# Optimization experiments

Hardware: AMD Instinct MI355X
Metric: run time of the kernel (lower is better)

## Reference

```python
import jax, jax.numpy as jnp
from jax import lax
import numpy as np

B, T, D = 1024, 64, 512   # batch, obs_len, input_size
HD = 512                  # hidden_size
L = 3                     # n_layers
FN = 64                   # num_filters
OH = 1                    # output_horizon
ATTN_LEN = T - 1          # conv kernel height
FEAT = HD                 # feat_size = attn_size - filter_size + 1, filter_size=1


def setup_inputs() -> dict:
    key = jax.random.key(0)
    ks = jax.random.split(key, 12)
    s = 0.02
    x = jax.random.normal(ks[0], (B, T, D), dtype=jnp.float32)
    # stacked LSTM weights (input_size == hidden_size so layer-0 stacks cleanly)
    W_ih = jax.random.normal(ks[1], (L, 4 * HD, HD), dtype=jnp.float32) * s
    W_hh = jax.random.normal(ks[2], (L, 4 * HD, HD), dtype=jnp.float32) * s
    b_ih = jax.random.normal(ks[3], (L, 4 * HD), dtype=jnp.float32) * s
    b_hh = jax.random.normal(ks[4], (L, 4 * HD), dtype=jnp.float32) * s
    # TPA: Conv2d(1, FN, (ATTN_LEN, 1)) in torch layout [FN, 1, ATTN_LEN, 1]
    conv_W = jax.random.normal(ks[5], (FN, 1, ATTN_LEN, 1), dtype=jnp.float32) * s
    conv_b = jax.random.normal(ks[6], (FN,), dtype=jnp.float32) * s
    lin1_W = jax.random.normal(ks[7], (FN, HD), dtype=jnp.float32) * s
    lin1_b = jax.random.normal(ks[8], (FN,), dtype=jnp.float32) * s
    lin2_W = jax.random.normal(ks[9], (HD, HD + FN), dtype=jnp.float32) * s
    lin2_b = jnp.zeros((HD,), dtype=jnp.float32)
    out_W = jax.random.normal(ks[10], (OH, HD), dtype=jnp.float32) * s
    out_b = jnp.zeros((OH,), dtype=jnp.float32)
    return dict(x=x, W_ih=W_ih, W_hh=W_hh, b_ih=b_ih, b_hh=b_hh,
                conv_W=conv_W, conv_b=conv_b, lin1_W=lin1_W, lin1_b=lin1_b,
                lin2_W=lin2_W, lin2_b=lin2_b, out_W=out_W, out_b=out_b)


def _lstm_last_layer_hs(x, W_ih, W_hh, b_ih, b_hh):
    """Run L-layer LSTM over time, return last-layer hidden per step [T,B,HD]."""
    h0 = jnp.zeros((L, B, HD), x.dtype)
    c0 = jnp.zeros((L, B, HD), x.dtype)

    def step(carry, xt):
        h, c = carry  # [L,B,HD]
        inp = xt
        hs, cs = [], []
        for l in range(L):  # small fixed layer count
            gates = inp @ W_ih[l].T + h[l] @ W_hh[l].T + b_ih[l] + b_hh[l]
            i, f, g, o = jnp.split(gates, 4, axis=-1)  # torch gate order i,f,g,o
            cl = jax.nn.sigmoid(f) * c[l] + jax.nn.sigmoid(i) * jnp.tanh(g)
            hl = jax.nn.sigmoid(o) * jnp.tanh(cl)
            hs.append(hl)
            cs.append(cl)
            inp = hl
        return (jnp.stack(hs), jnp.stack(cs)), hs[-1]

    _, ys = lax.scan(step, (h0, c0), jnp.swapaxes(x, 0, 1))
    return ys  # [T,B,HD]


def reference(x, W_ih, W_hh, b_ih, b_hh, conv_W, conv_b,
              lin1_W, lin1_b, lin2_W, lin2_b, out_W, out_b):
    ys = _lstm_last_layer_hs(x, W_ih, W_hh, b_ih, b_hh)   # [T,B,HD]
    htt = ys[-1]                                          # [B,HD] final hidden
    H = jax.nn.relu(jnp.swapaxes(ys[:-1], 0, 1))          # [B,T-1,HD]

    # Conv2d(1,FN,(T-1,1)) over [B,1,T-1,HD]: contracts the time axis only
    kW = conv_W[:, 0, :, 0]                               # [FN,T-1]
    conv_bcf = jnp.einsum('btf,ct->bcf', H, kW) + conv_b[:, None]  # [B,FN,FEAT]
    # torch .view(-1, feat_size, filter_num) on contiguous [B,FN,1,FEAT]
    conv_vecs = jax.nn.relu(conv_bcf.reshape(B, FEAT, FN))         # [B,FEAT,FN]

    w = htt @ lin1_W.T + lin1_b                           # [B,FN]
    s = jnp.sum(conv_vecs * w[:, None, :], axis=2)        # [B,FEAT]
    alpha = jax.nn.sigmoid(s)
    v = jnp.sum(alpha[:, :, None] * conv_vecs, axis=1)    # [B,FN]

    concat = jnp.concatenate([htt, v], axis=1)            # [B,HD+FN]
    new_ht = concat @ lin2_W.T + lin2_b                   # [B,HD]
    ypred = (new_ht @ out_W.T + out_b)[:, :, None]        # [B,OH,1]
    return ypred
```

## Files before the change

### kernel.cpp

```cpp
#include <hip/hip_runtime.h>
#include <hip/hip_bf16.h>


typedef short v8s __attribute__((ext_vector_type(8)));
typedef float v4f __attribute__((ext_vector_type(4)));
typedef __hip_bfloat16 bf16;

#define B_   1024
#define T_   64
#define D_   512
#define HD_  512

__device__ __forceinline__ float sigm(float v) { return 1.0f / (1.0f + __expf(-v)); }
__device__ __forceinline__ float tanh_(float v) { return 2.0f / (1.0f + __expf(-2.0f * v)) - 1.0f; }
__device__ __forceinline__ float b2f(bf16 v) { return __bfloat162float(v); }
__device__ __forceinline__ float bu2f(ushort u) {
  union { unsigned i; float f; } x; x.i = ((unsigned)u) << 16; return x.f;
}

__device__ __forceinline__ void cvt_store8(ushort* dst, const float* src) {
  float4 a = *(const float4*)src;
  float4 b = *(const float4*)(src + 4);
  bf16 h[8] = {__float2bfloat16(a.x), __float2bfloat16(a.y),
               __float2bfloat16(a.z), __float2bfloat16(a.w),
               __float2bfloat16(b.x), __float2bfloat16(b.y),
               __float2bfloat16(b.z), __float2bfloat16(b.w)};
  *(uint4*)dst = *(const uint4*)h;
}

__device__ __forceinline__ void glds16(const bf16* g, ushort* l) {
  __builtin_amdgcn_global_load_lds(
      (const __attribute__((address_space(1))) void*)g,
      (__attribute__((address_space(3))) void*)l, 16, 0, 0);
}

constexpr size_t SZ_YS = (size_t)T_ * B_ * HD_ * 2;
constexpr size_t SZ_HB = (size_t)2 * 2 * B_ * HD_ * 2;
constexpr size_t SZ_CB = (size_t)3 * B_ * HD_ * 4;
constexpr size_t SZ_ZP = (size_t)B_ * HD_ * 2;
constexpr size_t SZ_WV = (size_t)B_ * 64 * 4;
constexpr size_t SZ_VB = (size_t)B_ * 64 * 4;
constexpr size_t SZ_WB = (size_t)3 * 2048 * 1024 * 2;
constexpr size_t SZ_KT = (size_t)64 * 64 * 2;
constexpr size_t SZ_FW = (size_t)640 * 4;
constexpr size_t SZ_XB = (size_t)T_ * B_ * D_ * 2;
constexpr size_t O_YS = 0;
constexpr size_t O_HB = O_YS + SZ_YS;
constexpr size_t O_CB = O_HB + SZ_HB;
constexpr size_t O_ZP = O_CB + SZ_CB;
constexpr size_t O_WV = O_ZP + SZ_ZP;
constexpr size_t O_VB = O_WV + SZ_WV;
constexpr size_t O_WB = O_VB + SZ_VB;
constexpr size_t O_KT = O_WB + SZ_WB;
constexpr size_t O_FW = O_KT + SZ_KT;
constexpr size_t O_XB = O_FW + SZ_FW;

__global__ __launch_bounds__(256) void prep_w(const float* __restrict__ Wih,
                                              const float* __restrict__ Whh,
                                              bf16* __restrict__ Wbuf) {
  int tf = blockIdx.x * 256 + threadIdx.x;
  int group = tf >> 10;
  int layer = group >> 8, rem = group & 255;
  int nt = rem >> 4, ch = rem & 15;
  int li = tf & 1023;
  int frag = li >> 6, lane = li & 63;
  int nb = frag >> 1, kk = frag & 1;
  int c = lane & 15, q = lane >> 4;
  int half = nb >> 2, gate = nb & 3;
  int j = nt * 32 + half * 16 + c;
  int R = gate * 512 + j;
  int k = (ch & 7) * 64 + kk * 32 + q * 8;
  const float* src = ((ch < 8) ? Wih : Whh) + ((size_t)layer * 2048 + R) * 512 + k;
  cvt_store8((ushort*)(Wbuf + (size_t)tf * 8), src);
}

__global__ __launch_bounds__(256) void prep_x(const float* __restrict__ x,
                                              bf16* __restrict__ xb) {
  int idx = blockIdx.x * 256 + threadIdx.x;
  int d8 = idx & 63;
  int bt = idx >> 6;
  int b = bt & 1023, t = bt >> 10;
  cvt_store8((ushort*)(xb + ((size_t)t * B_ + b) * D_ + d8 * 8),
             x + ((size_t)b * T_ + t) * D_ + d8 * 8);
}

__global__ __launch_bounds__(256) void prep_kt(const float* __restrict__ convW,
                                               bf16* __restrict__ kT) {
  int idx = blockIdx.x * 256 + threadIdx.x;
  int t = idx >> 6, c = idx & 63;
  kT[idx] = __float2bfloat16(t < 63 ? convW[c * 63 + t] : 0.f);
}

__global__ __launch_bounds__(64) void prep_fw(const float* __restrict__ lin2W,
                                              const float* __restrict__ lin2b,
                                              const float* __restrict__ outW,
                                              const float* __restrict__ outb,
                                              float* __restrict__ fw) {
  const int blk = blockIdx.x, tid = threadIdx.x;
  if (blk < 9) {
    const int k = blk * 64 + tid;
    float a = 0.f;
    for (int j = 0; j < 512; ++j) a += outW[j] * lin2W[(size_t)j * 576 + k];
    fw[k] = a;
  } else {
    float a = 0.f;
    for (int j = tid; j < 512; j += 64) a += outW[j] * lin2b[j];
    for (int m = 1; m < 64; m <<= 1) a += __shfl_xor(a, m);
    if (tid == 0) fw[576] = a + outb[0];
  }
}

__global__ __launch_bounds__(512, 6) void lstm_stage(
    const bf16* __restrict__ xb, const bf16* __restrict__ Wbuf,
    const float* __restrict__ bih, const float* __restrict__ bhh,
    bf16* __restrict__ ys, bf16* __restrict__ hbuf, float* __restrict__ cbuf,
    const bf16* __restrict__ zp, int s, int llo) {
  __shared__ ushort As[2][4096];
  __shared__ ushort Bs[2][8192];

  const int layer = llo + (blockIdx.x >> 8);
  const int tile = blockIdx.x & 255;
  const int t = s - layer;
  const int mt = tile >> 4, nt = tile & 15;
  const int b0 = mt << 6;
  const int p = s & 1;

  bf16* hw = (layer < 2) ? hbuf + ((size_t)p * 2 + layer) * (B_ * HD_)
                         : ys + (size_t)t * (B_ * HD_);
  const bf16* srcA0 = (layer == 0)
      ? xb + (size_t)t * (B_ * D_)
      : hbuf + ((size_t)(p ^ 1) * 2 + (layer - 1)) * (B_ * HD_);
  const bf16* srcA1 = (layer < 2)
      ? hbuf + ((size_t)(p ^ 1) * 2 + layer) * (B_ * HD_)
      : ((t == 0) ? zp : ys + (size_t)(t - 1) * (B_ * HD_));
  const bf16* Wb = Wbuf + ((size_t)layer * 16 + nt) * 16 * 8192;

  const int tid = threadIdx.x, lane = tid & 63, w = tid >> 6;
  const int c = lane & 15, q = lane >> 4;
  const int wm = w >> 1, wn = w & 1;

  v4f acc[4];
#pragma unroll
  for (int ni = 0; ni < 4; ++ni) acc[ni] = v4f{0.f, 0.f, 0.f, 0.f};

  auto STAGE = [&](int ch, int pb) {
    const int kof = (ch & 7) * 64;
    const bf16* wsrc = Wb + (size_t)ch * 8192;
    const bf16* sA = (ch < 8) ? srcA0 : srcA1;
#pragma unroll
    for (int i = 0; i < 3; ++i) {
      int idx = w * 3 + i;
      if (idx < 16) {
        glds16(wsrc + idx * 512 + lane * 8, &Bs[pb][idx * 512]);
      } else {
        int f = idx - 16, mb = f >> 1, k2 = f & 1;
        glds16(sA + (size_t)(b0 + mb * 16 + c) * HD_ + kof + k2 * 32 + q * 8,
               &As[pb][f * 512]);
      }
    }
  };

  STAGE(0, 0);
  __syncthreads();

  for (int ch = 0; ch < 16; ++ch) {
    const int pb = ch & 1;
    if (ch < 15) STAGE(ch + 1, pb ^ 1);
    __builtin_amdgcn_s_setprio(1);
#pragma unroll
    for (int kk = 0; kk < 2; ++kk) {
      v8s af = *(const v8s*)&As[pb][(wm * 2 + kk) * 512 + lane * 8];
#pragma unroll
      for (int ni = 0; ni < 4; ++ni) {
        v8s bfr = *(const v8s*)&Bs[pb][((wn * 4 + ni) * 2 + kk) * 512 + lane * 8];
        acc[ni] = __builtin_amdgcn_mfma_f32_16x16x32_bf16(af, bfr, acc[ni], 0, 0, 0);
      }
    }
    __builtin_amdgcn_s_setprio(0);
    __syncthreads();
  }

  float* cl = cbuf + (size_t)layer * (B_ * HD_);
  const size_t bb = (size_t)layer * 2048;
  const int j = nt * 32 + wn * 16 + c;
  float bsum[4];
#pragma unroll
  for (int g4 = 0; g4 < 4; ++g4)
    bsum[g4] = bih[bb + g4 * 512 + j] + bhh[bb + g4 * 512 + j];
#pragma unroll
  for (int r = 0; r < 4; ++r) {
    const int b = b0 + wm * 16 + q * 4 + r;
    float iv = acc[0][r] + bsum[0];
    float fv = acc[1][r] + bsum[1];
    float gv = acc[2][r] + bsum[2];
    float ov = acc[3][r] + bsum[3];
    size_t off = (size_t)b * HD_ + j;
    float cprev = cl[off];
    float cn = sigm(fv) * cprev + sigm(iv) * tanh_(gv);
    float hn = sigm(ov) * tanh_(cn);
    cl[off] = cn;
    hw[off] = __float2bfloat16(hn);
  }
}

__global__ __launch_bounds__(64) void k0_lin1(const bf16* __restrict__ ys,
                                              const float* __restrict__ lin1W,
                                              const float* __restrict__ lin1b,
                                              float* __restrict__ wv) {
  __shared__ float htt[HD_];
  const int b = blockIdx.x, tid = threadIdx.x;
  for (int i = tid; i < HD_; i += 64)
    htt[i] = b2f(ys[((size_t)(T_ - 1) * B_ + b) * HD_ + i]);
  __syncthreads();
  float a = lin1b[tid];
  const float* wr = lin1W + (size_t)tid * HD_;
  for (int k = 0; k < HD_; k += 4) {
    float4 w4 = *(const float4*)(wr + k);
    a += htt[k] * w4.x + htt[k + 1] * w4.y + htt[k + 2] * w4.z + htt[k + 3] * w4.w;
  }
  wv[(size_t)b * 64 + tid] = a;
}

__global__ __launch_bounds__(256) void k1_attn(const bf16* __restrict__ ys,
                                               const bf16* __restrict__ kTb,
                                               const float* __restrict__ convb,
                                               const float* __restrict__ wv,
                                               float* __restrict__ vbuf) {
  __shared__ ushort HsL[63 * 512];
  __shared__ ushort kTL[64 * 64];
  __shared__ float wsh[64];
  __shared__ float cbs[64];
  const int b = blockIdx.x;
  const int tid = threadIdx.x, lane = tid & 63, w = tid >> 6;

  for (int idx = tid; idx < 63 * 64; idx += 256) {
    int t = idx >> 6, c8 = idx & 63;
    v8s h = *(const v8s*)(ys + ((size_t)t * B_ + b) * HD_ + c8 * 8);
    v8s r;
#pragma unroll
    for (int e = 0; e < 8; ++e) r[e] = (h[e] & (short)0x8000) ? (short)0 : h[e];
    *(v8s*)&HsL[t * 512 + c8 * 8] = r;
  }
  for (int idx = tid; idx < 512; idx += 256)
    *(v8s*)&kTL[idx * 8] = *(const v8s*)(kTb + idx * 8);
  if (tid < 64) { wsh[tid] = wv[(size_t)b * 64 + tid]; cbs[tid] = convb[tid]; }
  __syncthreads();

  const int ci = lane >> 3, fi = lane & 7;
#pragma unroll
  for (int fgi = 0; fgi < 2; ++fgi) {
    const int fg = w * 2 + fgi, f0 = fg << 6;
    float acc[8][8];
#pragma unroll
    for (int i = 0; i < 8; ++i)
#pragma unroll
      for (int jx = 0; jx < 8; ++jx) acc[i][jx] = 0.f;
    for (int t = 0; t < 63; ++t) {
      v8s k8 = *(const v8s*)&kTL[t * 64 + ci * 8];
      v8s h8 = *(const v8s*)&HsL[t * 512 + f0 + fi * 8];
      float av[8], hv[8];
#pragma unroll
      for (int e = 0; e < 8; ++e) { av[e] = bu2f((ushort)k8[e]); hv[e] = bu2f((ushort)h8[e]); }
#pragma unroll
      for (int i = 0; i < 8; ++i)
#pragma unroll
        for (int jx = 0; jx < 8; ++jx) acc[i][jx] += av[i] * hv[jx];
    }
#pragma unroll
    for (int i = 0; i < 8; ++i)
#pragma unroll
      for (int jx = 0; jx < 8; ++jx)
        acc[i][jx] = fmaxf(acc[i][jx] + cbs[ci * 8 + i], 0.f);

    float vp[8];
#pragma unroll
    for (int jx = 0; jx < 8; ++jx) vp[jx] = 0.f;
#pragma unroll
    for (int i = 0; i < 8; ++i) {
      float sp = 0.f;
#pragma unroll
      for (int jx = 0; jx < 8; ++jx) sp += acc[i][jx] * wsh[fi * 8 + jx];
      sp += __shfl_xor(sp, 1); sp += __shfl_xor(sp, 2); sp += __shfl_xor(sp, 4);
      float al = sigm(sp);
#pragma unroll
      for (int jx = 0; jx < 8; ++jx) vp[jx] += al * acc[i][jx];
    }
#pragma unroll
    for (int jx = 0; jx < 8; ++jx) {
      vp[jx] += __shfl_xor(vp[jx], 8);
      vp[jx] += __shfl_xor(vp[jx], 16);
      vp[jx] += __shfl_xor(vp[jx], 32);
    }
    if (ci == 0)
#pragma unroll
      for (int jx = 0; jx < 8; ++jx)
        atomicAdd(&vbuf[(size_t)b * 64 + fi * 8 + jx], vp[jx]);
  }
}

__global__ __launch_bounds__(64) void k3_out(const bf16* __restrict__ ys,
                                             const float* __restrict__ vbuf,
                                             const float* __restrict__ fw,
                                             float* __restrict__ out) {
  const int b = blockIdx.x, tid = threadIdx.x;
  v8s h = *(const v8s*)(ys + ((size_t)(T_ - 1) * B_ + b) * HD_ + tid * 8);
  const float4 w4a = *(const float4*)(fw + tid * 8);
  const float4 w4b = *(const float4*)(fw + tid * 8 + 4);
  float a = bu2f((ushort)h[0]) * w4a.x + bu2f((ushort)h[1]) * w4a.y +
            bu2f((ushort)h[2]) * w4a.z + bu2f((ushort)h[3]) * w4a.w +
            bu2f((ushort)h[4]) * w4b.x + bu2f((ushort)h[5]) * w4b.y +
            bu2f((ushort)h[6]) * w4b.z + bu2f((ushort)h[7]) * w4b.w;
  a += vbuf[(size_t)b * 64 + tid] * fw[512 + tid];
  for (int m = 1; m < 64; m <<= 1) a += __shfl_xor(a, m);
  if (tid == 0) out[b] = a + fw[576];
}

extern "C" void kernel_launch(void* const* d_in, const int* in_sizes, int n_in,
                              void* d_out, int out_size, void* d_ws, size_t ws_size,
                              hipStream_t stream) {
  const float* x     = (const float*)d_in[0];
  const float* Wih   = (const float*)d_in[1];
  const float* Whh   = (const float*)d_in[2];
  const float* bih   = (const float*)d_in[3];
  const float* bhh   = (const float*)d_in[4];
  const float* convW = (const float*)d_in[5];
  const float* convb = (const float*)d_in[6];
  const float* lin1W = (const float*)d_in[7];
  const float* lin1b = (const float*)d_in[8];
  const float* lin2W = (const float*)d_in[9];
  const float* lin2b = (const float*)d_in[10];
  const float* outW  = (const float*)d_in[11];
  const float* outb  = (const float*)d_in[12];

  char* ws = (char*)d_ws;
  bf16*  ys   = (bf16*)(ws + O_YS);
  bf16*  hbuf = (bf16*)(ws + O_HB);
  float* cbuf = (float*)(ws + O_CB);
  bf16*  zp   = (bf16*)(ws + O_ZP);
  float* wv   = (float*)(ws + O_WV);
  float* vbuf = (float*)(ws + O_VB);
  bf16*  Wbuf = (bf16*)(ws + O_WB);
  bf16*  kTb  = (bf16*)(ws + O_KT);
  float* fwv  = (float*)(ws + O_FW);
  bf16*  xb   = (bf16*)(ws + O_XB);

  hipMemsetAsync(hbuf, 0, SZ_HB, stream);
  hipMemsetAsync(cbuf, 0, SZ_CB, stream);
  hipMemsetAsync((void*)zp, 0, SZ_ZP, stream);
  hipMemsetAsync(vbuf, 0, SZ_VB, stream);

  prep_w<<<3072, 256, 0, stream>>>(Wih, Whh, Wbuf);
  prep_x<<<16384, 256, 0, stream>>>(x, xb);
  prep_kt<<<16, 256, 0, stream>>>(convW, kTb);
  prep_fw<<<10, 64, 0, stream>>>(lin2W, lin2b, outW, outb, fwv);

  for (int s = 0; s < T_ + 3 - 1; ++s) {
    int llo = (s > T_ - 1) ? (s - (T_ - 1)) : 0;
    int lhi = (s < 2) ? s : 2;
    int cnt = lhi - llo + 1;
    lstm_stage<<<cnt * 256, 512, 0, stream>>>(xb, Wbuf, bih, bhh, ys, hbuf,
                                              cbuf, zp, s, llo);
  }

  k0_lin1<<<B_, 64, 0, stream>>>(ys, lin1W, lin1b, wv);
  k1_attn<<<B_, 256, 0, stream>>>(ys, kTb, convb, wv, vbuf);
  k3_out<<<B_, 64, 0, stream>>>(ys, vbuf, fwv, (float*)d_out);
}
```

Baseline: 1.968 ms.

## Compute TPA conv contraction in k1_attn with bf16 MFMA and swizzled LDS

The attention kernel's time-axis conv contraction, previously done as scalar FP32 FMAs over LDS, now runs on 16x16x32 bf16 MFMA instructions. To supply this, the hidden states are transposed into an XOR-swizzled LDS layout with time packed in pairs per feature, meant to avoid bank conflicts. The conv weight is prepared in channel-major order so it can be loaded straight into A fragments. The bias, ReLU, sigmoid scoring and weighted reduction are redone on the MFMA accumulator layout. This adds complex fragment and swizzle indexing, and it only speeds up the post-LSTM stage, which is a small part of the total runtime.

```diff
diff --git a/kernel.cpp b/kernel.cpp
--- a/kernel.cpp
+++ b/kernel.cpp
@@ -41,7 +41,7 @@
 constexpr size_t SZ_WV = (size_t)B_ * 64 * 4;
 constexpr size_t SZ_VB = (size_t)B_ * 64 * 4;
 constexpr size_t SZ_WB = (size_t)3 * 2048 * 1024 * 2;
-constexpr size_t SZ_KT = (size_t)64 * 64 * 2;
+constexpr size_t SZ_KC = (size_t)64 * 64 * 2;
 constexpr size_t SZ_FW = (size_t)640 * 4;
 constexpr size_t SZ_XB = (size_t)T_ * B_ * D_ * 2;
 constexpr size_t O_YS = 0;
@@ -51,8 +51,8 @@
 constexpr size_t O_WV = O_ZP + SZ_ZP;
 constexpr size_t O_VB = O_WV + SZ_WV;
 constexpr size_t O_WB = O_VB + SZ_VB;
-constexpr size_t O_KT = O_WB + SZ_WB;
-constexpr size_t O_FW = O_KT + SZ_KT;
+constexpr size_t O_KC = O_WB + SZ_WB;
+constexpr size_t O_FW = O_KC + SZ_KC;
 constexpr size_t O_XB = O_FW + SZ_FW;
 
 __global__ __launch_bounds__(256) void prep_w(const float* __restrict__ Wih,
@@ -84,11 +84,11 @@
              x + ((size_t)b * T_ + t) * D_ + d8 * 8);
 }
 
-__global__ __launch_bounds__(256) void prep_kt(const float* __restrict__ convW,
-                                               bf16* __restrict__ kT) {
+__global__ __launch_bounds__(256) void prep_kc(const float* __restrict__ convW,
+                                               bf16* __restrict__ kC) {
   int idx = blockIdx.x * 256 + threadIdx.x;
-  int t = idx >> 6, c = idx & 63;
-  kT[idx] = __float2bfloat16(t < 63 ? convW[c * 63 + t] : 0.f);
+  int c = idx >> 6, t = idx & 63;
+  kC[idx] = __float2bfloat16(t < 63 ? convW[c * 63 + t] : 0.f);
 }
 
 __global__ __launch_bounds__(64) void prep_fw(const float* __restrict__ lin2W,
@@ -222,79 +222,118 @@
 }
 
 __global__ __launch_bounds__(256) void k1_attn(const bf16* __restrict__ ys,
-                                               const bf16* __restrict__ kTb,
+                                               const bf16* __restrict__ kCb,
                                                const float* __restrict__ convb,
-                                               const float* __restrict__ wv,
+                                               const float* __restrict__ wvg,
                                                float* __restrict__ vbuf) {
-  __shared__ ushort HsL[63 * 512];
-  __shared__ ushort kTL[64 * 64];
-  __shared__ float wsh[64];
-  __shared__ float cbs[64];
+  __shared__ ushort Ht[32768];
   const int b = blockIdx.x;
   const int tid = threadIdx.x, lane = tid & 63, w = tid >> 6;
-
-  for (int idx = tid; idx < 63 * 64; idx += 256) {
-    int t = idx >> 6, c8 = idx & 63;
-    v8s h = *(const v8s*)(ys + ((size_t)t * B_ + b) * HD_ + c8 * 8);
-    v8s r;
-#pragma unroll
-    for (int e = 0; e < 8; ++e) r[e] = (h[e] & (short)0x8000) ? (short)0 : h[e];
-    *(v8s*)&HsL[t * 512 + c8 * 8] = r;
-  }
-  for (int idx = tid; idx < 512; idx += 256)
-    *(v8s*)&kTL[idx * 8] = *(const v8s*)(kTb + idx * 8);
-  if (tid < 64) { wsh[tid] = wv[(size_t)b * 64 + tid]; cbs[tid] = convb[tid]; }
+  const int l15 = lane & 15, q = lane >> 4;
+  char* HtB = (char*)Ht;
+
+  for (int idx = tid; idx < 2048; idx += 256) {
+    int f8 = (idx & 7) | (((idx >> 6) & 7) << 3);
+    int t2 = ((idx >> 3) & 7) | ((idx >> 9) << 3);
+    int t = t2 * 2;
+    v8s ha = *(const v8s*)(ys + ((size_t)t * B_ + b) * HD_ + f8 * 8);
+    v8s hb;
+    if (t2 == 31) {
+      hb = v8s{0, 0, 0, 0, 0, 0, 0, 0};
+    } else {
+      hb = *(const v8s*)(ys + ((size_t)(t + 1) * B_ + b) * HD_ + f8 * 8);
+    }
+#pragma unroll
+    for (int e = 0; e < 8; ++e) {
+      ushort lo = (ha[e] & (short)0x8000) ? (ushort)0 : (ushort)ha[e];
+      ushort hi = (hb[e] & (short)0x8000) ? (ushort)0 : (ushort)hb[e];
+      int f = f8 * 8 + e;
+      int chunk = ((t >> 3) ^ (f & 7) ^ ((f >> 3) & 7)) & 7;
+      *(unsigned*)(HtB + f * 128 + chunk * 16 + (t & 7) * 2) =
+          (unsigned)lo | ((unsigned)hi << 16);
+    }
+  }
   __syncthreads();
 
-  const int ci = lane >> 3, fi = lane & 7;
-#pragma unroll
-  for (int fgi = 0; fgi < 2; ++fgi) {
-    const int fg = w * 2 + fgi, f0 = fg << 6;
-    float acc[8][8];
-#pragma unroll
-    for (int i = 0; i < 8; ++i)
-#pragma unroll
-      for (int jx = 0; jx < 8; ++jx) acc[i][jx] = 0.f;
-    for (int t = 0; t < 63; ++t) {
-      v8s k8 = *(const v8s*)&kTL[t * 64 + ci * 8];
-      v8s h8 = *(const v8s*)&HsL[t * 512 + f0 + fi * 8];
-      float av[8], hv[8];
-#pragma unroll
-      for (int e = 0; e < 8; ++e) { av[e] = bu2f((ushort)k8[e]); hv[e] = bu2f((ushort)h8[e]); }
-#pragma unroll
-      for (int i = 0; i < 8; ++i)
-#pragma unroll
-        for (int jx = 0; jx < 8; ++jx) acc[i][jx] += av[i] * hv[jx];
+  v8s af[4][2];
+#pragma unroll
+  for (int mi = 0; mi < 4; ++mi)
+#pragma unroll
+    for (int kk = 0; kk < 2; ++kk)
+      af[mi][kk] = *(const v8s*)(kCb + (mi * 16 + l15) * 64 + kk * 32 + q * 8);
+
+  v4f acc[4][8];
+#pragma unroll
+  for (int mi = 0; mi < 4; ++mi)
+#pragma unroll
+    for (int ni = 0; ni < 8; ++ni) acc[mi][ni] = v4f{0.f, 0.f, 0.f, 0.f};
+
+#pragma unroll
+  for (int ni = 0; ni < 8; ++ni) {
+    const int f = w * 128 + ni * 16 + l15;
+#pragma unroll
+    for (int kk = 0; kk < 2; ++kk) {
+      const int t0 = kk * 32 + q * 8;
+      const int chunk = ((t0 >> 3) ^ (f & 7) ^ ((f >> 3) & 7)) & 7;
+      v8s bf = *(const v8s*)(HtB + f * 128 + chunk * 16);
+#pragma unroll
+      for (int mi = 0; mi < 4; ++mi)
+        acc[mi][ni] = __builtin_amdgcn_mfma_f32_16x16x32_bf16(af[mi][kk], bf, acc[mi][ni], 0, 0, 0);
     }
-#pragma unroll
-    for (int i = 0; i < 8; ++i)
-#pragma unroll
-      for (int jx = 0; jx < 8; ++jx)
-        acc[i][jx] = fmaxf(acc[i][jx] + cbs[ci * 8 + i], 0.f);
-
-    float vp[8];
-#pragma unroll
-    for (int jx = 0; jx < 8; ++jx) vp[jx] = 0.f;
-#pragma unroll
-    for (int i = 0; i < 8; ++i) {
-      float sp = 0.f;
-#pragma unroll
-      for (int jx = 0; jx < 8; ++jx) sp += acc[i][jx] * wsh[fi * 8 + jx];
-      sp += __shfl_xor(sp, 1); sp += __shfl_xor(sp, 2); sp += __shfl_xor(sp, 4);
-      float al = sigm(sp);
-#pragma unroll
-      for (int jx = 0; jx < 8; ++jx) vp[jx] += al * acc[i][jx];
-    }
-#pragma unroll
-    for (int jx = 0; jx < 8; ++jx) {
-      vp[jx] += __shfl_xor(vp[jx], 8);
-      vp[jx] += __shfl_xor(vp[jx], 16);
-      vp[jx] += __shfl_xor(vp[jx], 32);
-    }
-    if (ci == 0)
-#pragma unroll
-      for (int jx = 0; jx < 8; ++jx)
-        atomicAdd(&vbuf[(size_t)b * 64 + fi * 8 + jx], vp[jx]);
+  }
+
+  float cb[4][4];
+#pragma unroll
+  for (int mi = 0; mi < 4; ++mi)
+#pragma unroll
+    for (int r = 0; r < 4; ++r) cb[mi][r] = convb[mi * 16 + q * 4 + r];
+  float wl[4];
+#pragma unroll
+  for (int nl = 0; nl < 4; ++nl) wl[nl] = wvg[(size_t)b * 64 + nl * 16 + l15];
+
+#pragma unroll
+  for (int mi = 0; mi < 4; ++mi)
+#pragma unroll
+    for (int ni = 0; ni < 8; ++ni)
+#pragma unroll
+      for (int r = 0; r < 4; ++r)
+        acc[mi][ni][r] = fmaxf(acc[mi][ni][r] + cb[mi][r], 0.f);
+
+  float al[4][4][2];
+#pragma unroll
+  for (int mi = 0; mi < 4; ++mi)
+#pragma unroll
+    for (int r = 0; r < 4; ++r)
+#pragma unroll
+      for (int nh = 0; nh < 2; ++nh) {
+        float s = 0.f;
+#pragma unroll
+        for (int nl = 0; nl < 4; ++nl)
+          s += acc[mi][nh * 4 + nl][r] * wl[nl];
+        s += __shfl_xor(s, 1); s += __shfl_xor(s, 2);
+        s += __shfl_xor(s, 4); s += __shfl_xor(s, 8);
+        al[mi][r][nh] = sigm(s);
+      }
+
+  float vp[4];
+#pragma unroll
+  for (int nl = 0; nl < 4; ++nl) {
+    float v = 0.f;
+#pragma unroll
+    for (int mi = 0; mi < 4; ++mi)
+#pragma unroll
+      for (int r = 0; r < 4; ++r)
+#pragma unroll
+      for (int nh = 0; nh < 2; ++nh)
+        v += al[mi][r][nh] * acc[mi][nh * 4 + nl][r];
+    v += __shfl_xor(v, 16);
+    v += __shfl_xor(v, 32);
+    vp[nl] = v;
+  }
+  if (lane < 16) {
+#pragma unroll
+    for (int nl = 0; nl < 4; ++nl)
+      atomicAdd(&vbuf[(size_t)b * 64 + nl * 16 + l15], vp[nl]);
   }
 }
 
@@ -340,7 +379,7 @@
   float* wv   = (float*)(ws + O_WV);
   float* vbuf = (float*)(ws + O_VB);
   bf16*  Wbuf = (bf16*)(ws + O_WB);
-  bf16*  kTb  = (bf16*)(ws + O_KT);
+  bf16*  kCb  = (bf16*)(ws + O_KC);
   float* fwv  = (float*)(ws + O_FW);
   bf16*  xb   = (bf16*)(ws + O_XB);
 
@@ -351,7 +390,7 @@
 
   prep_w<<<3072, 256, 0, stream>>>(Wih, Whh, Wbuf);
   prep_x<<<16384, 256, 0, stream>>>(x, xb);
-  prep_kt<<<16, 256, 0, stream>>>(convW, kTb);
+  prep_kc<<<16, 256, 0, stream>>>(convW, kCb);
   prep_fw<<<10, 64, 0, stream>>>(lin2W, lin2b, outW, outb, fwv);
 
   for (int s = 0; s < T_ + 3 - 1; ++s) {
@@ -363,6 +402,6 @@
   }
 
   k0_lin1<<<B_, 64, 0, stream>>>(ys, lin1W, lin1b, wv);
-  k1_attn<<<B_, 256, 0, stream>>>(ys, kTb, convb, wv, vbuf);
+  k1_attn<<<B_, 256, 0, stream>>>(ys, kCb, convb, wv, vbuf);
   k3_out<<<B_, 64, 0, stream>>>(ys, vbuf, fwv, (float*)d_out);
 }
```

Result: no change. 1.985 ms (+0.9%).
